# Kernel optimization log

Hardware: AMD Instinct MI355X
Metric: run time of the kernel (lower is better)

Reference implementation:

```python
import jax, jax.numpy as jnp
import numpy as np

B, S, E, H, D = 2, 2048, 1024, 16, 64  # batch, seq(=max_seq_len), embed_dim, heads, atten_dim


def setup_inputs() -> dict:
    key = jax.random.key(0)
    ks = jax.random.split(key, 9)
    s = 0.02
    return {
        "x": jax.random.normal(ks[0], (B, S, E), jnp.float32),
        "Wq": jax.random.normal(ks[1], (H, E, D), jnp.float32) * s,
        "Wk": jax.random.normal(ks[2], (H, E, D), jnp.float32) * s,
        "Wv": jax.random.normal(ks[3], (H, E, D), jnp.float32) * s,
        "bq": jax.random.normal(ks[4], (H, D), jnp.float32) * s,
        "bk": jax.random.normal(ks[5], (H, D), jnp.float32) * s,
        "bv": jax.random.normal(ks[6], (H, D), jnp.float32) * s,
        "Wp": jax.random.normal(ks[7], (H * D, E), jnp.float32) * s,
        "bp": jax.random.normal(ks[8], (E,), jnp.float32) * s,
    }


def reference(x, Wq, Wk, Wv, bq, bk, bv, Wp, bp):
    scale = jnp.sqrt(jnp.float32(D))
    # per-head projections, all heads at once: [B,H,S,D]
    q = jnp.einsum("bse,hed->bhsd", x, Wq) + bq[:, None, :]
    k = jnp.einsum("bse,hed->bhsd", x, Wk) + bk[:, None, :]
    v = jnp.einsum("bse,hed->bhsd", x, Wv) + bv[:, None, :]
    # causal scores [B,H,S,S], additive -inf mask above diagonal (as in the buffer)
    score = jnp.einsum("bhsd,bhtd->bhst", q, k) / scale
    mask = jnp.triu(jnp.full((S, S), -jnp.inf, jnp.float32), k=1)
    score = score + mask
    probs = jax.nn.softmax(score, axis=-1)
    attn = jnp.einsum("bhst,bhtd->bhsd", probs, v)
    # concat heads -> [B,S,H*D], then projection + ReLU
    concat = attn.transpose(0, 2, 1, 3).reshape(B, S, H * D)
    out = jax.nn.relu(concat @ Wp + bp)
    return out
```

## Files before the change

### kernel.cpp

```cpp
#include <hip/hip_runtime.h>

#define S_LEN 2048
#define E_DIM 1024
#define H_NUM 16
#define D_DIM 64

typedef unsigned short u16;
using bf16x8 = __attribute__((ext_vector_type(8))) short;
using f32x4  = __attribute__((ext_vector_type(4))) float;
using f32x16 = __attribute__((ext_vector_type(16))) float;

#define MFMA16(A, B, C) __builtin_amdgcn_mfma_f32_16x16x32_bf16(A, B, C, 0, 0, 0)
#define MFMA32(A, B, C) __builtin_amdgcn_mfma_f32_32x32x16_bf16(A, B, C, 0, 0, 0)
#define QSCALE 0.18033688011112042f

__device__ __forceinline__ u16 f2bf(float f) {
    unsigned u = __float_as_uint(f);
    u += 0x7fffu + ((u >> 16) & 1u);
    return (u16)(u >> 16);
}
__device__ __forceinline__ f32x4 fzero4() { f32x4 z; z[0]=0.f; z[1]=0.f; z[2]=0.f; z[3]=0.f; return z; }
__device__ __forceinline__ f32x16 fzero16() {
    f32x16 z;
    #pragma unroll
    for (int i = 0; i < 16; i++) z[i] = 0.f;
    return z;
}

__device__ __forceinline__ unsigned cvtpk(float a, float b) {
    unsigned r;
    asm("v_cvt_pk_bf16_f32 %0, %1, %2" : "=v"(r) : "v"(a), "v"(b));
    return r;
}
__device__ __forceinline__ float fexp2(float x) {
#if __has_builtin(__builtin_amdgcn_exp2f)
    return __builtin_amdgcn_exp2f(x);
#else
    float r; asm("v_exp_f32 %0, %1" : "=v"(r) : "v"(x)); return r;
#endif
}
__device__ __forceinline__ float frcp(float x) {
#if __has_builtin(__builtin_amdgcn_rcpf)
    return __builtin_amdgcn_rcpf(x);
#else
    float r; asm("v_rcp_f32 %0, %1" : "=v"(r) : "v"(x)); return r;
#endif
}

__device__ __forceinline__ void gll16(const u16* g, u16* l) {
    __builtin_amdgcn_global_load_lds(
        (const __attribute__((address_space(1))) void*)g,
        (__attribute__((address_space(3))) void*)l, 16, 0, 0);
}

__device__ __forceinline__ void stage64(const u16* __restrict__ g, int gstride,
                                        u16* l, int wave, int lane) {
    #pragma unroll
    for (int i = 0; i < 2; i++) {
        const int r  = wave * 16 + i * 8 + (lane >> 3);
        const int sl = (lane & 7) ^ (r & 7);
        gll16(g + (size_t)r * gstride + sl * 8, l + (wave * 16 + i * 8) * 64);
    }
}
__device__ __forceinline__ bf16x8 ldswz(const u16* t, int rr, int hh, int quad) {
    const int sl = ((hh << 2) + quad) ^ (rr & 7);
    return *(const bf16x8*)(t + rr * 64 + sl * 8);
}
__device__ __forceinline__ bf16x8 ldfr(const u16* t, int rr, int sl) {
    return *(const bf16x8*)(t + rr * 64 + ((sl ^ (rr & 7)) * 8));
}

__device__ __forceinline__ void cvt_t_tile(const float* __restrict__ bin, u16* __restrict__ bout,
                                           int R, int C, int r0, int c0) {
    __shared__ float t[64][65];
    const int tid = threadIdx.x;
    const int lr = tid >> 2, lc = (tid & 3) * 16;

    const float* src = bin + (size_t)(r0 + lr) * C + c0 + lc;
    #pragma unroll
    for (int j = 0; j < 4; j++) {
        float4 f = *(const float4*)(src + j * 4);
        t[lr][lc + j * 4 + 0] = f.x; t[lr][lc + j * 4 + 1] = f.y;
        t[lr][lc + j * 4 + 2] = f.z; t[lr][lc + j * 4 + 3] = f.w;
    }
    __syncthreads();

    u16* dst = bout + (size_t)(c0 + lr) * R + r0 + lc;
    u16 vals[16];
    #pragma unroll
    for (int i = 0; i < 16; i++) vals[i] = f2bf(t[lc + i][lr]);
    uint4 pa, pb;
    pa.x = vals[0] | (vals[1] << 16);  pa.y = vals[2] | (vals[3] << 16);
    pa.z = vals[4] | (vals[5] << 16);  pa.w = vals[6] | (vals[7] << 16);
    pb.x = vals[8] | (vals[9] << 16);  pb.y = vals[10] | (vals[11] << 16);
    pb.z = vals[12] | (vals[13] << 16); pb.w = vals[14] | (vals[15] << 16);
    *(uint4*)dst = pa;
    *(uint4*)(dst + 8) = pb;
}

__global__ __launch_bounds__(256) void cvt_all(
    const float* __restrict__ x, u16* __restrict__ xb, int n,
    const float* __restrict__ Wq, const float* __restrict__ Wk, const float* __restrict__ Wv,
    u16* __restrict__ wqt, u16* __restrict__ wkt, u16* __restrict__ wvt,
    const float* __restrict__ Wp, u16* __restrict__ wpt)
{
    const int bid = blockIdx.x;
    if (bid < 4096) {
        int i4 = (bid * 256 + threadIdx.x) * 4;
        if (i4 < n) {
            float4 f = *(const float4*)(x + i4);
            unsigned lo = (unsigned)f2bf(f.x) | ((unsigned)f2bf(f.y) << 16);
            unsigned hi = (unsigned)f2bf(f.z) | ((unsigned)f2bf(f.w) << 16);
            uint2 p; p.x = lo; p.y = hi;
            *(uint2*)(xb + i4) = p;
        }
    } else if (bid < 4096 + 768) {
        const int t  = bid - 4096;
        const int z  = t >> 4;
        const int ry = t & 15;
        const int which = z >> 4, bh = z & 15;
        const float* in = (which == 0) ? Wq : (which == 1) ? Wk : Wv;
        u16* outp = (which == 0) ? wqt : (which == 1) ? wkt : wvt;
        cvt_t_tile(in + (size_t)bh * E_DIM * D_DIM, outp + (size_t)bh * E_DIM * D_DIM,
                   E_DIM, D_DIM, ry * 64, 0);
    } else {
        const int t = bid - (4096 + 768);
        cvt_t_tile(Wp, wpt, H_NUM * D_DIM, E_DIM, (t >> 4) * 64, (t & 15) * 64);
    }
}

__global__ __launch_bounds__(128, 2) void qkv_gemm(
    const u16* __restrict__ xb, const u16* __restrict__ wcat,
    const float* __restrict__ bq, const float* __restrict__ bk, const float* __restrict__ bv,
    u16* __restrict__ oq, u16* __restrict__ okk, u16* __restrict__ ov)
{
    const int m0 = blockIdx.x * 128;
    const int n0 = blockIdx.y * 128;

    __shared__ u16 As[3][64 * 64];
    __shared__ u16 Bs[3][64 * 64];

    const int tid  = threadIdx.x;
    const int wave = tid >> 6, lane = tid & 63, quad = lane >> 4, l16 = lane & 15;

    f32x4 acc[8][4];
    #pragma unroll
    for (int j = 0; j < 8; j++)
        #pragma unroll
        for (int mi = 0; mi < 4; mi++) acc[j][mi] = fzero4();

#define STAGE(K0, BUF)                                                               \
    _Pragma("unroll")                                                                \
    for (int i = 0; i < 2; i++) {                                                    \
        const int r  = wave * 32 + i * 8 + (lane >> 3);           \
        const int s  = (lane & 7) ^ (r & 7);                      \
        const int mr = r + ((s >> 2) << 6);                      \
        const int kc = (s & 3) * 8;                              \
        gll16(xb   + (size_t)(m0 + mr) * E_DIM + (K0) + kc,                          \
              &As[BUF][(wave * 32 + i * 8) * 64]);                                   \
        gll16(wcat + (size_t)(n0 + mr) * E_DIM + (K0) + kc,                          \
              &Bs[BUF][(wave * 32 + i * 8) * 64]);                                   \
        const int r2  = wave * 32 + 16 + i * 8 + (lane >> 3);                        \
        const int s2  = (lane & 7) ^ (r2 & 7);                                       \
        const int mr2 = r2 + ((s2 >> 2) << 6);                                       \
        const int kc2 = (s2 & 3) * 8;                                                \
        gll16(xb   + (size_t)(m0 + mr2) * E_DIM + (K0) + kc2,                        \
              &As[BUF][(wave * 32 + 16 + i * 8) * 64]);                              \
        gll16(wcat + (size_t)(n0 + mr2) * E_DIM + (K0) + kc2,                        \
              &Bs[BUF][(wave * 32 + 16 + i * 8) * 64]);                              \
    }

    STAGE(0, 0);
    STAGE(32, 1);

    for (int kt = 0; kt < 32; kt++) {
        if (kt < 31) { asm volatile("s_waitcnt vmcnt(8) lgkmcnt(0)" ::: "memory"); }
        else         { asm volatile("s_waitcnt vmcnt(0) lgkmcnt(0)" ::: "memory"); }
        __builtin_amdgcn_s_barrier();
        if (kt < 30) {
            const int kn = (kt + 2) * 32;
            const int bn = (kt + 2) % 3;
            STAGE(kn, bn);
        }
        const u16* Ac = As[kt % 3];
        const u16* Bc = Bs[kt % 3];

        bf16x8 af[4];
        #pragma unroll
        for (int mi = 0; mi < 4; mi++) {
            const int row = mi * 16 + l16;
            af[mi] = *(const bf16x8*)(&Ac[row * 64 + ((((wave << 2) + quad)) ^ (row & 7)) * 8]);
        }
        __builtin_amdgcn_s_setprio(1);
        #pragma unroll
        for (int j = 0; j < 8; j++) {
            const int row = (j & 3) * 16 + l16;
            bf16x8 bfv = *(const bf16x8*)(&Bc[row * 64 +
                              ((((j >> 2) << 2) + quad) ^ (row & 7)) * 8]);
            #pragma unroll
            for (int mi = 0; mi < 4; mi++)
                acc[j][mi] = MFMA16(af[mi], bfv, acc[j][mi]);
        }
        __builtin_amdgcn_s_setprio(0);
    }
#undef STAGE

    const int t = n0 >> 10;
    if (t < 2) {
        const float scl = (t == 0) ? QSCALE : 1.0f;
        const float* bias = (t == 0) ? bq : bk;
        u16* dst = (t == 0) ? oq : okk;
        #pragma unroll
        for (int j = 0; j < 8; j++) {
            const int n = n0 + j * 16 + l16;
            const int h = (n >> 6) & 15, d = n & 63;
            float bia = bias[h * D_DIM + d];
            #pragma unroll
            for (int mi = 0; mi < 4; mi++) {
                #pragma unroll
                for (int r = 0; r < 4; r++) {
                    int m = m0 + wave * 64 + mi * 16 + quad * 4 + r;
                    int b = m >> 11, s = m & 2047;
                    dst[((size_t)(b * H_NUM + h) * S_LEN + s) * D_DIM + d] =
                        f2bf((acc[j][mi][r] + bia) * scl);
                }
            }
        }
    } else {
        const int b  = m0 >> 11, s0 = m0 & 2047;
        const int h0 = (n0 >> 6) & 15;
        u16* Tb0 = &As[0][0];
        u16* Tb1 = &Bs[0][0];
        #pragma unroll
        for (int pass = 0; pass < 2; ++pass) {
            __syncthreads();
            if (wave == pass) {
                #pragma unroll
                for (int j = 0; j < 8; j++) {
                    const int n = n0 + j * 16 + l16;
                    const int d = n & 63, hh = (n >> 6) & 15;
                    const float bia = bv[hh * D_DIM + d];
                    u16* Tb = (j < 4) ? Tb0 : Tb1;
                    const int nl = (j & 3) * 16 + l16;
                    #pragma unroll
                    for (int mi = 0; mi < 4; mi++) {
                        uint2 pk;
                        pk.x = cvtpk(acc[j][mi][0] + bia, acc[j][mi][1] + bia);
                        pk.y = cvtpk(acc[j][mi][2] + bia, acc[j][mi][3] + bia);
                        *(uint2*)(&Tb[nl * 72 + mi * 16 + quad * 4]) = pk;
                    }
                }
            }
            __syncthreads();
            #pragma unroll
            for (int g = 0; g < 8; ++g) {
                const int rowi = g * 16 + (tid >> 3);
                const int ml = (tid & 7) * 8;
                const u16* srcp = (rowi < 64 ? Tb0 : Tb1) + (rowi & 63) * 72 + ml;
                const int hh = h0 + (rowi >> 6), d = rowi & 63;
                u16* dstp = ov + ((size_t)(b * H_NUM + hh) * D_DIM + d) * S_LEN
                               + s0 + pass * 64 + ml;
                *(uint4*)dstp = *(const uint4*)srcp;
            }
        }
    }
}

__global__ __launch_bounds__(256, 2) void attn_fwd(
    const u16* __restrict__ q, const u16* __restrict__ k, const u16* __restrict__ vt,
    u16* __restrict__ concat)
{
    const int bid  = blockIdx.x;
    const int halfg = bid >> 8;
    const int pi   = (bid & 255) >> 5;
    const int p    = halfg ? (15 - pi) : pi;
    const int g    = bid & 31;
    const int hd   = g & 15;
    const int bb   = g >> 4;
    const int qa = p, qb = 31 - p;

    const size_t headoff = (size_t)(bb * H_NUM + hd) * S_LEN * D_DIM;
    const u16* qptr = q  + headoff;
    const u16* kptr = k  + headoff;
    const u16* vptr = vt + headoff;

    __shared__ u16 Ks[3][64 * 64];
    __shared__ u16 Vts[3][64 * 64];
    __shared__ float Lsb[2][2][32];
    __shared__ float Lsa[2][2][32];

    const int tid  = threadIdx.x;
    const int wave = tid >> 6, lane = tid & 63;
    const int l32 = lane & 31, hh = lane >> 5;
    const int qhalf = wave & 1, kh = wave >> 1;

    stage64(qptr + (size_t)qb * 64 * D_DIM, D_DIM, Ks[0],  wave, lane);
    stage64(qptr + (size_t)qa * 64 * D_DIM, D_DIM, Vts[0], wave, lane);
    __syncthreads();

    bf16x8 qfb[4], qfa[4];
    {
        const int row = qhalf * 32 + l32;
        #pragma unroll
        for (int c = 0; c < 4; c++) {
            qfb[c] = ldfr(&Ks[0][0],  row, c * 2 + hh);
            qfa[c] = ldfr(&Vts[0][0], row, c * 2 + hh);
        }
    }
    __syncthreads();

    stage64(kptr, D_DIM, Ks[0],  wave, lane);
    stage64(vptr, S_LEN, Vts[0], wave, lane);
    stage64(kptr + (size_t)64 * D_DIM, D_DIM, Ks[1],  wave, lane);
    stage64(vptr + 64,                 S_LEN, Vts[1], wave, lane);

    f32x16 ob0 = fzero16(), ob1 = fzero16();
    f32x16 oa0 = fzero16(), oa1 = fzero16();
    float lsb = 0.f, lsa = 0.f;
    const int qgb = qb * 64 + qhalf * 32 + l32;
    const int qga = qa * 64 + qhalf * 32 + l32;
    const int kkbase = kh * 32 + 4 * hh;

#define BUILD_PA(PE, D0, D1)                                                      \
        {                                                                         \
            unsigned X0 = cvtpk(PE[0], PE[1]),   X1 = cvtpk(PE[2], PE[3]);        \
            unsigned Y0 = cvtpk(PE[4], PE[5]),   Y1 = cvtpk(PE[6], PE[7]);        \
            asm("v_permlane32_swap_b32 %0, %1" : "+v"(X0), "+v"(Y0));             \
            asm("v_permlane32_swap_b32 %0, %1" : "+v"(X1), "+v"(Y1));             \
            int4 f0; f0.x = (int)X0; f0.y = (int)X1; f0.z = (int)Y0; f0.w = (int)Y1; \
            D0 = *(bf16x8*)&f0;                                                   \
            unsigned Z0 = cvtpk(PE[8], PE[9]),   Z1 = cvtpk(PE[10], PE[11]);      \
            unsigned W0 = cvtpk(PE[12], PE[13]), W1 = cvtpk(PE[14], PE[15]);      \
            asm("v_permlane32_swap_b32 %0, %1" : "+v"(Z0), "+v"(W0));             \
            asm("v_permlane32_swap_b32 %0, %1" : "+v"(Z1), "+v"(W1));             \
            int4 f1; f1.x = (int)Z0; f1.y = (int)Z1; f1.z = (int)W0; f1.w = (int)W1; \
            D1 = *(bf16x8*)&f1;                                                   \
        }

    for (int kt = 0; kt <= qb; kt++) {
        if (kt < qb) { asm volatile("s_waitcnt vmcnt(4) lgkmcnt(0)" ::: "memory"); }
        else         { asm volatile("s_waitcnt vmcnt(0) lgkmcnt(0)" ::: "memory"); }
        __builtin_amdgcn_s_barrier();
        if (kt + 2 <= qb) {
            stage64(kptr + (size_t)(kt + 2) * 64 * D_DIM, D_DIM, Ks[(kt + 2) % 3],  wave, lane);
            stage64(vptr + (kt + 2) * 64,                 S_LEN, Vts[(kt + 2) % 3], wave, lane);
        }
        const u16* Kc = &Ks[kt % 3][0];
        const u16* Vc = &Vts[kt % 3][0];

        {
            f32x16 s = fzero16();
            __builtin_amdgcn_s_setprio(1);
            #pragma unroll
            for (int c = 0; c < 4; c++) {
                bf16x8 ak = ldfr(Kc, kh * 32 + l32, c * 2 + hh);
                s = MFMA32(ak, qfb[c], s);
            }
            __builtin_amdgcn_s_setprio(0);

            float pe[16];
            if (kt == qb) {
                #pragma unroll
                for (int r = 0; r < 16; r++) {
                    const int kkg = kt * 64 + kkbase + (r & 3) + 8 * (r >> 2);
                    pe[r] = (kkg > qgb) ? 0.f : fexp2(s[r]);
                }
            } else {
                #pragma unroll
                for (int r = 0; r < 16; r++) pe[r] = fexp2(s[r]);
            }
            #pragma unroll
            for (int r = 0; r < 16; r++) lsb += pe[r];

            bf16x8 pa0, pa1;
            BUILD_PA(pe, pa0, pa1);

            __builtin_amdgcn_s_setprio(1);
            {
                bf16x8 v00 = ldfr(Vc, l32,      (2 * kh    ) * 2 + hh);
                bf16x8 v10 = ldfr(Vc, 32 + l32, (2 * kh    ) * 2 + hh);
                bf16x8 v01 = ldfr(Vc, l32,      (2 * kh + 1) * 2 + hh);
                bf16x8 v11 = ldfr(Vc, 32 + l32, (2 * kh + 1) * 2 + hh);
                ob0 = MFMA32(pa0, v00, ob0);
                ob1 = MFMA32(pa0, v10, ob1);
                ob0 = MFMA32(pa1, v01, ob0);
                ob1 = MFMA32(pa1, v11, ob1);
            }
            __builtin_amdgcn_s_setprio(0);
        }

        if (kt <= qa) {
            f32x16 s = fzero16();
            __builtin_amdgcn_s_setprio(1);
            #pragma unroll
            for (int c = 0; c < 4; c++) {
                bf16x8 ak = ldfr(Kc, kh * 32 + l32, c * 2 + hh);
                s = MFMA32(ak, qfa[c], s);
            }
            __builtin_amdgcn_s_setprio(0);

            float pe[16];
            if (kt == qa) {
                #pragma unroll
                for (int r = 0; r < 16; r++) {
                    const int kkg = kt * 64 + kkbase + (r & 3) + 8 * (r >> 2);
                    pe[r] = (kkg > qga) ? 0.f : fexp2(s[r]);
                }
            } else {
                #pragma unroll
                for (int r = 0; r < 16; r++) pe[r] = fexp2(s[r]);
            }
            #pragma unroll
            for (int r = 0; r < 16; r++) lsa += pe[r];

            bf16x8 pa0, pa1;
            BUILD_PA(pe, pa0, pa1);

            __builtin_amdgcn_s_setprio(1);
            {
                bf16x8 v00 = ldfr(Vc, l32,      (2 * kh    ) * 2 + hh);
                bf16x8 v10 = ldfr(Vc, 32 + l32, (2 * kh    ) * 2 + hh);
                bf16x8 v01 = ldfr(Vc, l32,      (2 * kh + 1) * 2 + hh);
                bf16x8 v11 = ldfr(Vc, 32 + l32, (2 * kh + 1) * 2 + hh);
                oa0 = MFMA32(pa0, v00, oa0);
                oa1 = MFMA32(pa0, v10, oa1);
                oa0 = MFMA32(pa1, v01, oa0);
                oa1 = MFMA32(pa1, v11, oa1);
            }
            __builtin_amdgcn_s_setprio(0);
        }
    }
#undef BUILD_PA

    __syncthreads();

    lsb += __shfl_xor(lsb, 32);
    lsa += __shfl_xor(lsa, 32);
    if (hh == 0) {
        Lsb[kh][qhalf][l32] = lsb;
        Lsa[kh][qhalf][l32] = lsa;
    }

    float* Rb = (float*)(&Ks[0][0])  + qhalf * 2048;
    float* Ra = (float*)(&Vts[0][0]) + qhalf * 2048;

    if (kh == 1) {
        #pragma unroll
        for (int r = 0; r < 16; r++) {
            const int qlr = (r & 3) + 8 * (r >> 2) + 4 * hh;
            Rb[qlr * 64 + l32]      = ob0[r];
            Rb[qlr * 64 + 32 + l32] = ob1[r];
            Ra[qlr * 64 + l32]      = oa0[r];
            Ra[qlr * 64 + 32 + l32] = oa1[r];
        }
    }
    __syncthreads();

    if (kh == 0) {
        #pragma unroll
        for (int r = 0; r < 16; r++) {
            const int qlr = (r & 3) + 8 * (r >> 2) + 4 * hh;
            const float lib = frcp(Lsb[0][qhalf][qlr] + Lsb[1][qhalf][qlr]);
            const float lia = frcp(Lsa[0][qhalf][qlr] + Lsa[1][qhalf][qlr]);
            const float vb0 = ob0[r] + Rb[qlr * 64 + l32];
            const float vb1 = ob1[r] + Rb[qlr * 64 + 32 + l32];
            const float va0 = oa0[r] + Ra[qlr * 64 + l32];
            const float va1 = oa1[r] + Ra[qlr * 64 + 32 + l32];
            const int qrb = qb * 64 + qhalf * 32 + qlr;
            const int qra = qa * 64 + qhalf * 32 + qlr;
            u16* db = concat + ((size_t)(bb * S_LEN + qrb)) * E_DIM + hd * D_DIM;
            u16* da = concat + ((size_t)(bb * S_LEN + qra)) * E_DIM + hd * D_DIM;
            db[l32]      = f2bf(vb0 * lib);
            db[32 + l32] = f2bf(vb1 * lib);
            da[l32]      = f2bf(va0 * lia);
            da[32 + l32] = f2bf(va1 * lia);
        }
    }
}

__global__ __launch_bounds__(256, 2) void out_proj(
    const u16* __restrict__ concat, const u16* __restrict__ wpt,
    const float* __restrict__ bp, float* __restrict__ out)
{
    const int bid = blockIdx.x;
    const int mt  = (bid & 7) * 8 + ((bid >> 3) & 7);
    const int nt0 = bid >> 6;
    const int m0 = mt * 64;
    const int n0 = nt0 * 128;

    __shared__ u16 As[2][64 * 64];
    __shared__ u16 Bs[2][128 * 64];

    const int tid  = threadIdx.x;
    const int wave = tid >> 6, lane = tid & 63, quad = lane >> 4, l16 = lane & 15;
    const int mh = wave >> 1, nh = wave & 1;

    f32x4 acc[4][2];
    #pragma unroll
    for (int j = 0; j < 4; j++)
        #pragma unroll
        for (int mi = 0; mi < 2; mi++) acc[j][mi] = fzero4();

    stage64(concat + (size_t)m0 * E_DIM, E_DIM, As[0], wave, lane);
    stage64(wpt + (size_t)n0 * E_DIM,        E_DIM, Bs[0],           wave, lane);
    stage64(wpt + (size_t)(n0 + 64) * E_DIM, E_DIM, Bs[0] + 64 * 64, wave, lane);

    for (int kt = 0; kt < 16; kt++) {
        __syncthreads();
        if (kt < 15) {
            const int k0 = (kt + 1) * 64;
            u16* an = As[(kt + 1) & 1];
            u16* bn = Bs[(kt + 1) & 1];
            stage64(concat + (size_t)m0 * E_DIM + k0, E_DIM, an, wave, lane);
            stage64(wpt + (size_t)n0 * E_DIM + k0,        E_DIM, bn,           wave, lane);
            stage64(wpt + (size_t)(n0 + 64) * E_DIM + k0, E_DIM, bn + 64 * 64, wave, lane);
        }
        const u16* Ac = As[kt & 1];
        const u16* Bc = Bs[kt & 1];

        #pragma unroll
        for (int kq = 0; kq < 2; kq++) {
            bf16x8 af[2];
            #pragma unroll
            for (int mi = 0; mi < 2; mi++)
                af[mi] = ldswz(Ac, mh * 32 + mi * 16 + l16, kq, quad);
            __builtin_amdgcn_s_setprio(1);
            #pragma unroll
            for (int j = 0; j < 4; j++) {
                bf16x8 bfv = ldswz(Bc, nh * 64 + j * 16 + l16, kq, quad);
                #pragma unroll
                for (int mi = 0; mi < 2; mi++)
                    acc[j][mi] = MFMA16(af[mi], bfv, acc[j][mi]);
            }
            __builtin_amdgcn_s_setprio(0);
        }
    }

    #pragma unroll
    for (int j = 0; j < 4; j++) {
        int n = n0 + nh * 64 + j * 16 + l16;
        float bia = bp[n];
        #pragma unroll
        for (int mi = 0; mi < 2; mi++) {
            #pragma unroll
            for (int r = 0; r < 4; r++) {
                int m = m0 + mh * 32 + mi * 16 + quad * 4 + r;
                out[(size_t)m * E_DIM + n] = fmaxf(acc[j][mi][r] + bia, 0.f);
            }
        }
    }
}

extern "C" void kernel_launch(void* const* d_in, const int* in_sizes, int n_in,
                              void* d_out, int out_size, void* d_ws, size_t ws_size,
                              hipStream_t stream)
{
    (void)in_sizes; (void)n_in; (void)out_size; (void)ws_size;
    const float* x  = (const float*)d_in[0];
    const float* Wq = (const float*)d_in[1];
    const float* Wk = (const float*)d_in[2];
    const float* Wv = (const float*)d_in[3];
    const float* bq = (const float*)d_in[4];
    const float* bk = (const float*)d_in[5];
    const float* bv = (const float*)d_in[6];
    const float* Wp = (const float*)d_in[7];
    const float* bp = (const float*)d_in[8];
    float* out = (float*)d_out;

    const size_t QKV_ELEMS = (size_t)2 * H_NUM * S_LEN * D_DIM;
    const size_t W_ELEMS   = (size_t)H_NUM * E_DIM * D_DIM;

    u16* q   = (u16*)d_ws;
    u16* k   = q   + QKV_ELEMS;
    u16* v   = k   + QKV_ELEMS;
    u16* cc  = v   + QKV_ELEMS;
    u16* xb  = cc  + QKV_ELEMS;
    u16* wqt = xb  + QKV_ELEMS;
    u16* wkt = wqt + W_ELEMS;
    u16* wvt = wkt + W_ELEMS;
    u16* wpt = wvt + W_ELEMS;

    cvt_all<<<dim3(4096 + 768 + 256), 256, 0, stream>>>(
        x, xb, (int)QKV_ELEMS, Wq, Wk, Wv, wqt, wkt, wvt, Wp, wpt);

    qkv_gemm<<<dim3(32, 24), 128, 0, stream>>>(xb, wqt, bq, bk, bv, q, k, v);
    attn_fwd<<<dim3(512), 256, 0, stream>>>(q, k, v, cc);
    out_proj<<<dim3(512), 256, 0, stream>>>(cc, wpt, bp, out);
}
```

Measured before the change: 173.3 us.

## Process 128-key chunks per iteration with double-buffered K/V staging

The attention loop now stages 128 keys per step into a two-slot double buffer instead of 64 keys into a three-slot ring. Each key-half wave group handles its own 64-key half as two 32-key sub-tiles. This halves the number of barriers and loop iterations and gives each wave more MFMA work per sync. In exchange, the hand-tuned vmcnt waits are replaced by plain __syncthreads, so prefetch overlap is shallower and load latency may be exposed. LDS use grows from 6 to 8 tiles, which could pressure occupancy at 2 blocks per CU.

```diff
diff --git a/kernel.cpp b/kernel.cpp
--- a/kernel.cpp
+++ b/kernel.cpp
@@ -284,8 +284,8 @@
     const u16* kptr = k  + headoff;
     const u16* vptr = vt + headoff;
 
-    __shared__ u16 Ks[3][64 * 64];
-    __shared__ u16 Vts[3][64 * 64];
+    __shared__ u16 Ks[2][2][64 * 64];
+    __shared__ u16 Vts[2][2][64 * 64];
     __shared__ float Lsb[2][2][32];
     __shared__ float Lsa[2][2][32];
 
@@ -294,8 +294,8 @@
     const int l32 = lane & 31, hh = lane >> 5;
     const int qhalf = wave & 1, kh = wave >> 1;
 
-    stage64(qptr + (size_t)qb * 64 * D_DIM, D_DIM, Ks[0],  wave, lane);
-    stage64(qptr + (size_t)qa * 64 * D_DIM, D_DIM, Vts[0], wave, lane);
+    stage64(qptr + (size_t)qb * 64 * D_DIM, D_DIM, Ks[0][0],  wave, lane);
+    stage64(qptr + (size_t)qa * 64 * D_DIM, D_DIM, Vts[0][0], wave, lane);
     __syncthreads();
 
     bf16x8 qfb[4], qfa[4];
@@ -303,23 +303,30 @@
         const int row = qhalf * 32 + l32;
         #pragma unroll
         for (int c = 0; c < 4; c++) {
-            qfb[c] = ldfr(&Ks[0][0],  row, c * 2 + hh);
-            qfa[c] = ldfr(&Vts[0][0], row, c * 2 + hh);
+            qfb[c] = ldfr(&Ks[0][0][0],  row, c * 2 + hh);
+            qfa[c] = ldfr(&Vts[0][0][0], row, c * 2 + hh);
         }
     }
     __syncthreads();
 
-    stage64(kptr, D_DIM, Ks[0],  wave, lane);
-    stage64(vptr, S_LEN, Vts[0], wave, lane);
-    stage64(kptr + (size_t)64 * D_DIM, D_DIM, Ks[1],  wave, lane);
-    stage64(vptr + 64,                 S_LEN, Vts[1], wave, lane);
+    const int nc_b = (qb + 2) >> 1;
+    const int nc_a = (qa + 2) >> 1;
+
+#define STAGE_KV(C, BUF)                                                              \
+    {                                                                                 \
+        stage64(kptr + (size_t)((C) * 128     ) * D_DIM, D_DIM, Ks[BUF][0],  wave, lane); \
+        stage64(kptr + (size_t)((C) * 128 + 64) * D_DIM, D_DIM, Ks[BUF][1],  wave, lane); \
+        stage64(vptr + (C) * 128,                        S_LEN, Vts[BUF][0], wave, lane); \
+        stage64(vptr + (C) * 128 + 64,                   S_LEN, Vts[BUF][1], wave, lane); \
+    }
+
+    STAGE_KV(0, 0);
 
     f32x16 ob0 = fzero16(), ob1 = fzero16();
     f32x16 oa0 = fzero16(), oa1 = fzero16();
     float lsb = 0.f, lsa = 0.f;
     const int qgb = qb * 64 + qhalf * 32 + l32;
     const int qga = qa * 64 + qhalf * 32 + l32;
-    const int kkbase = kh * 32 + 4 * hh;
 
 #define BUILD_PA(PE, D0, D1)                                                      \
         {                                                                         \
@@ -337,100 +344,104 @@
             D1 = *(bf16x8*)&f1;                                                   \
         }
 
-    for (int kt = 0; kt <= qb; kt++) {
-        if (kt < qb) { asm volatile("s_waitcnt vmcnt(4) lgkmcnt(0)" ::: "memory"); }
-        else         { asm volatile("s_waitcnt vmcnt(0) lgkmcnt(0)" ::: "memory"); }
-        __builtin_amdgcn_s_barrier();
-        if (kt + 2 <= qb) {
-            stage64(kptr + (size_t)(kt + 2) * 64 * D_DIM, D_DIM, Ks[(kt + 2) % 3],  wave, lane);
-            stage64(vptr + (kt + 2) * 64,                 S_LEN, Vts[(kt + 2) % 3], wave, lane);
-        }
-        const u16* Kc = &Ks[kt % 3][0];
-        const u16* Vc = &Vts[kt % 3][0];
-
-        {
-            f32x16 s = fzero16();
-            __builtin_amdgcn_s_setprio(1);
-            #pragma unroll
-            for (int c = 0; c < 4; c++) {
-                bf16x8 ak = ldfr(Kc, kh * 32 + l32, c * 2 + hh);
-                s = MFMA32(ak, qfb[c], s);
+    for (int c = 0; c < nc_b; c++) {
+        __syncthreads();
+        if (c + 1 < nc_b) STAGE_KV(c + 1, (c + 1) & 1);
+        const u16* Kc = Ks[c & 1][kh];
+        const u16* Vc = Vts[c & 1][kh];
+        const bool lastb = (c == nc_b - 1);
+        const bool doa   = (c < nc_a);
+        const bool lasta = (c == nc_a - 1);
+
+        #pragma unroll
+        for (int sub = 0; sub < 2; sub++) {
+            const int kkb = c * 128 + kh * 64 + sub * 32 + 4 * hh;
+
+            {
+                f32x16 s = fzero16();
+                __builtin_amdgcn_s_setprio(1);
+                #pragma unroll
+                for (int c4 = 0; c4 < 4; c4++) {
+                    bf16x8 ak = ldfr(Kc, sub * 32 + l32, c4 * 2 + hh);
+                    s = MFMA32(ak, qfb[c4], s);
+                }
+                __builtin_amdgcn_s_setprio(0);
+
+                float pe[16];
+                if (lastb) {
+                    #pragma unroll
+                    for (int r = 0; r < 16; r++) {
+                        const int kkg = kkb + (r & 3) + 8 * (r >> 2);
+                        pe[r] = (kkg > qgb) ? 0.f : fexp2(s[r]);
+                    }
+                } else {
+                    #pragma unroll
+                    for (int r = 0; r < 16; r++) pe[r] = fexp2(s[r]);
+                }
+                #pragma unroll
+                for (int r = 0; r < 16; r++) lsb += pe[r];
+
+                bf16x8 pa0, pa1;
+                BUILD_PA(pe, pa0, pa1);
+
+                __builtin_amdgcn_s_setprio(1);
+                {
+                    bf16x8 v00 = ldfr(Vc, l32,      sub * 4 + hh);
+                    bf16x8 v10 = ldfr(Vc, 32 + l32, sub * 4 + hh);
+                    bf16x8 v01 = ldfr(Vc, l32,      sub * 4 + 2 + hh);
+                    bf16x8 v11 = ldfr(Vc, 32 + l32, sub * 4 + 2 + hh);
+                    ob0 = MFMA32(pa0, v00, ob0);
+                    ob1 = MFMA32(pa0, v10, ob1);
+                    ob0 = MFMA32(pa1, v01, ob0);
+                    ob1 = MFMA32(pa1, v11, ob1);
+                }
+                __builtin_amdgcn_s_setprio(0);
             }
-            __builtin_amdgcn_s_setprio(0);
-
-            float pe[16];
-            if (kt == qb) {
+
+            if (doa) {
+                f32x16 s = fzero16();
+                __builtin_amdgcn_s_setprio(1);
                 #pragma unroll
-                for (int r = 0; r < 16; r++) {
-                    const int kkg = kt * 64 + kkbase + (r & 3) + 8 * (r >> 2);
-                    pe[r] = (kkg > qgb) ? 0.f : fexp2(s[r]);
-                }
-            } else {
+                for (int c4 = 0; c4 < 4; c4++) {
+                    bf16x8 ak = ldfr(Kc, sub * 32 + l32, c4 * 2 + hh);
+                    s = MFMA32(ak, qfa[c4], s);
+                }
+                __builtin_amdgcn_s_setprio(0);
+
+                float pe[16];
+                if (lasta) {
+                    #pragma unroll
+                    for (int r = 0; r < 16; r++) {
+                        const int kkg = kkb + (r & 3) + 8 * (r >> 2);
+                        pe[r] = (kkg > qga) ? 0.f : fexp2(s[r]);
+                    }
+                } else {
+                    #pragma unroll
+                    for (int r = 0; r < 16; r++) pe[r] = fexp2(s[r]);
+                }
                 #pragma unroll
-                for (int r = 0; r < 16; r++) pe[r] = fexp2(s[r]);
+                for (int r = 0; r < 16; r++) lsa += pe[r];
+
+                bf16x8 pa0, pa1;
+                BUILD_PA(pe, pa0, pa1);
+
+                __builtin_amdgcn_s_setprio(1);
+                {
+                    bf16x8 v00 = ldfr(Vc, l32,      sub * 4 + hh);
+                    bf16x8 v10 = ldfr(Vc, 32 + l32, sub * 4 + hh);
+                    bf16x8 v01 = ldfr(Vc, l32,      sub * 4 + 2 + hh);
+                    bf16x8 v11 = ldfr(Vc, 32 + l32, sub * 4 + 2 + hh);
+                    oa0 = MFMA32(pa0, v00, oa0);
+                    oa1 = MFMA32(pa0, v10, oa1);
+                    oa0 = MFMA32(pa1, v01, oa0);
+                    oa1 = MFMA32(pa1, v11, oa1);
+                }
+                __builtin_amdgcn_s_setprio(0);
             }
-            #pragma unroll
-            for (int r = 0; r < 16; r++) lsb += pe[r];
-
-            bf16x8 pa0, pa1;
-            BUILD_PA(pe, pa0, pa1);
-
-            __builtin_amdgcn_s_setprio(1);
-            {
-                bf16x8 v00 = ldfr(Vc, l32,      (2 * kh    ) * 2 + hh);
-                bf16x8 v10 = ldfr(Vc, 32 + l32, (2 * kh    ) * 2 + hh);
-                bf16x8 v01 = ldfr(Vc, l32,      (2 * kh + 1) * 2 + hh);
-                bf16x8 v11 = ldfr(Vc, 32 + l32, (2 * kh + 1) * 2 + hh);
-                ob0 = MFMA32(pa0, v00, ob0);
-                ob1 = MFMA32(pa0, v10, ob1);
-                ob0 = MFMA32(pa1, v01, ob0);
-                ob1 = MFMA32(pa1, v11, ob1);
-            }
-            __builtin_amdgcn_s_setprio(0);
-        }
-
-        if (kt <= qa) {
-            f32x16 s = fzero16();
-            __builtin_amdgcn_s_setprio(1);
-            #pragma unroll
-            for (int c = 0; c < 4; c++) {
-                bf16x8 ak = ldfr(Kc, kh * 32 + l32, c * 2 + hh);
-                s = MFMA32(ak, qfa[c], s);
-            }
-            __builtin_amdgcn_s_setprio(0);
-
-            float pe[16];
-            if (kt == qa) {
-                #pragma unroll
-                for (int r = 0; r < 16; r++) {
-                    const int kkg = kt * 64 + kkbase + (r & 3) + 8 * (r >> 2);
-                    pe[r] = (kkg > qga) ? 0.f : fexp2(s[r]);
-                }
-            } else {
-                #pragma unroll
-                for (int r = 0; r < 16; r++) pe[r] = fexp2(s[r]);
-            }
-            #pragma unroll
-            for (int r = 0; r < 16; r++) lsa += pe[r];
-
-            bf16x8 pa0, pa1;
-            BUILD_PA(pe, pa0, pa1);
-
-            __builtin_amdgcn_s_setprio(1);
-            {
-                bf16x8 v00 = ldfr(Vc, l32,      (2 * kh    ) * 2 + hh);
-                bf16x8 v10 = ldfr(Vc, 32 + l32, (2 * kh    ) * 2 + hh);
-                bf16x8 v01 = ldfr(Vc, l32,      (2 * kh + 1) * 2 + hh);
-                bf16x8 v11 = ldfr(Vc, 32 + l32, (2 * kh + 1) * 2 + hh);
-                oa0 = MFMA32(pa0, v00, oa0);
-                oa1 = MFMA32(pa0, v10, oa1);
-                oa0 = MFMA32(pa1, v01, oa0);
-                oa1 = MFMA32(pa1, v11, oa1);
-            }
-            __builtin_amdgcn_s_setprio(0);
         }
     }
 #undef BUILD_PA
+#undef STAGE_KV
 
     __syncthreads();
 
@@ -441,8 +452,8 @@
         Lsa[kh][qhalf][l32] = lsa;
     }
 
-    float* Rb = (float*)(&Ks[0][0])  + qhalf * 2048;
-    float* Ra = (float*)(&Vts[0][0]) + qhalf * 2048;
+    float* Rb = (float*)(&Ks[0][0][0])  + qhalf * 2048;
+    float* Ra = (float*)(&Vts[0][0][0]) + qhalf * 2048;
 
     if (kh == 1) {
         #pragma unroll
```

New measurement: 173.4 us. About the same (+0.1%).
